# Kernel tuning notes

Measured on AMD Instinct MI355X. Metric: run time of the kernel, lower is better.

The kernel has to match this reference:

```python
import jax, jax.numpy as jnp
import numpy as np

B, T, D = 64, 1024, 512

def setup_inputs() -> dict:
    key = jax.random.key(0)
    ks = jax.random.split(key, 5)
    s_in = 1.0 / np.sqrt(2 * D)
    s_m = 1.0 / np.sqrt(D)
    return {
        "x": jax.random.normal(ks[0], (B, T, D), dtype=jnp.float32),
        "tau_w": jax.random.normal(ks[1], (D, 2 * D), dtype=jnp.float32) * s_in,
        "tau_b": jax.random.normal(ks[2], (D,), dtype=jnp.float32) * s_in,
        "mem_w": jax.random.normal(ks[3], (D, D), dtype=jnp.float32) * s_m,
        "mem_b": jax.random.normal(ks[4], (D,), dtype=jnp.float32) * s_m,
        "threshold": jnp.asarray(0.5, dtype=jnp.float32),
    }

def reference(x, tau_w, tau_b, mem_w, mem_b, threshold):
    b, t, d = x.shape
    dt = x.dtype
    # tau_fc input is cat([xt, tau]); split weight into x-part and tau-part
    Wx = tau_w[:, :d]   # [D, D] acting on xt
    Wt = tau_w[:, d:]   # [D, D] acting on previous tau
    # precompute the parts that depend only on x (dropout=0 -> identity)
    xproj = jnp.einsum('btd,ed->bte', x, Wx) + tau_b      # tau_fc x-contribution
    m = jnp.einsum('btd,ed->bte', x, mem_w) + mem_b       # mem_fc(xt)

    def step(carry, inp):
        v, tau = carry
        xp_t, m_t = inp
        tau = jax.nn.sigmoid(xp_t + tau @ Wt.T)
        alpha = jnp.exp(-1.0 / (tau + 1e-6))
        v = alpha * v + (1.0 - alpha) * m_t
        s = (v >= threshold).astype(dt)
        v = v * (1.0 - s)
        return (v, tau), s

    v0 = jnp.zeros((b, d), dtype=dt)
    tau0 = jnp.ones((b, d), dtype=dt)
    (v, tau), spikes = jax.lax.scan(
        step, (v0, tau0),
        (jnp.swapaxes(xproj, 0, 1), jnp.swapaxes(m, 0, 1)))
    return jnp.swapaxes(spikes, 0, 1), tau, v
```

## Files before the change

kernel.cpp:

```cpp
#include <hip/hip_runtime.h>

#define BB 64
#define TT 1024
#define DD 512
#define BT (BB*TT)

#define SENT 0xFFFFFFFFFFFFFFFFULL
#define TAUG_WORDS (2ULL * 64 * 4 * 192)

typedef float f4 __attribute__((ext_vector_type(4)));

__global__ __launch_bounds__(256, 2) void gemm_kernel(
    const float* __restrict__ x, const float* __restrict__ tau_w,
    const float* __restrict__ tau_b, const float* __restrict__ mem_w,
    const float* __restrict__ mem_b, float* __restrict__ xp, float* __restrict__ mm)
{
    __shared__ float As[32][132];
    __shared__ float Bs[32][68];

    const int tid  = threadIdx.x;
    const int bt0  = blockIdx.x * 128;
    const bool isxp = (blockIdx.y < 8);
    const float* W       = isxp ? tau_w : mem_w;
    const int    wstride = isxp ? 1024 : 512;
    const int    e0      = isxp ? blockIdx.y * 64 : blockIdx.y * 64 - 512;
    const float* bias    = isxp ? tau_b : mem_b;
    float*       dst     = isxp ? xp : mm;

    const int tm = tid & 31, tn = tid >> 5;
    const int lr = tid >> 3, lc = tid & 7;

    float bias_r[8];
#pragma unroll
    for (int ni = 0; ni < 8; ni++) bias_r[ni] = bias[e0 + tn * 8 + ni];

    float acc[4][8] = {};
    float4 pa[4], pb[2];

#pragma unroll
    for (int j = 0; j < 4; j++)
        pa[j] = *(const float4*)(x + (size_t)(bt0 + lr + 32 * j) * DD + lc * 4);
#pragma unroll
    for (int j = 0; j < 2; j++)
        pb[j] = *(const float4*)(W + (size_t)(e0 + lr + 32 * j) * wstride + lc * 4);

    for (int kb = 0; kb < DD; kb += 32) {
#pragma unroll
        for (int j = 0; j < 4; j++) {
            As[lc * 4 + 0][lr + 32 * j] = pa[j].x;
            As[lc * 4 + 1][lr + 32 * j] = pa[j].y;
            As[lc * 4 + 2][lr + 32 * j] = pa[j].z;
            As[lc * 4 + 3][lr + 32 * j] = pa[j].w;
        }
#pragma unroll
        for (int j = 0; j < 2; j++) {
            Bs[lc * 4 + 0][lr + 32 * j] = pb[j].x;
            Bs[lc * 4 + 1][lr + 32 * j] = pb[j].y;
            Bs[lc * 4 + 2][lr + 32 * j] = pb[j].z;
            Bs[lc * 4 + 3][lr + 32 * j] = pb[j].w;
        }
        __syncthreads();
        if (kb + 32 < DD) {
#pragma unroll
            for (int j = 0; j < 4; j++)
                pa[j] = *(const float4*)(x + (size_t)(bt0 + lr + 32 * j) * DD + kb + 32 + lc * 4);
#pragma unroll
            for (int j = 0; j < 2; j++)
                pb[j] = *(const float4*)(W + (size_t)(e0 + lr + 32 * j) * wstride + kb + 32 + lc * 4);
        }
#pragma unroll
        for (int k = 0; k < 32; k++) {
            float4 av  = *(const float4*)&As[k][tm * 4];
            float4 bv0 = *(const float4*)&Bs[k][tn * 8];
            float4 bv1 = *(const float4*)&Bs[k][tn * 8 + 4];
            float a_[4] = {av.x, av.y, av.z, av.w};
            float b_[8] = {bv0.x, bv0.y, bv0.z, bv0.w, bv1.x, bv1.y, bv1.z, bv1.w};
#pragma unroll
            for (int mi = 0; mi < 4; mi++)
#pragma unroll
                for (int ni = 0; ni < 8; ni++)
                    acc[mi][ni] = fmaf(a_[mi], b_[ni], acc[mi][ni]);
        }
        __syncthreads();
    }

#pragma unroll
    for (int mi = 0; mi < 4; mi++) {
        const int row = bt0 + tm * 4 + mi;
        float o[8];
#pragma unroll
        for (int ni = 0; ni < 8; ni++) o[ni] = __fadd_rn(acc[mi][ni], bias_r[ni]);
        float4 s0 = {o[0], o[1], o[2], o[3]};
        float4 s1 = {o[4], o[5], o[6], o[7]};
        *(float4*)(dst + (size_t)row * DD + e0 + tn * 8)     = s0;
        *(float4*)(dst + (size_t)row * DD + e0 + tn * 8 + 4) = s1;
    }
}

__global__ __launch_bounds__(512, 1) void scan_kernel(
    const float* __restrict__ tau_w,
    float* __restrict__ xp_sp,
    const float* __restrict__ mm,
    const float* __restrict__ thrp,
    float* __restrict__ tau_out, float* __restrict__ v_out,
    unsigned long long* __restrict__ taug64)
{
    __shared__ float tau_lds[DD];
    __shared__ float partial[4][128];

    const int wg = blockIdx.x;
    const int b = wg >> 2, p = wg & 3;
    const int tid = threadIdx.x;
    const int w = tid >> 6, lane = tid & 63;
    const int c  = w & 3;
    const int le = ((w >> 2) << 6) + lane;
    const int ge = p * 128 + le;

    float wv[128];
    {
        const float4* wrow = (const float4*)(tau_w + (size_t)ge * 1024 + 512 + c * 128);
#pragma unroll
        for (int j = 0; j < 32; j++) {
            float4 t = wrow[j];
            wv[4 * j + 0] = t.x; wv[4 * j + 1] = t.y;
            wv[4 * j + 2] = t.z; wv[4 * j + 3] = t.w;
        }
    }
#pragma unroll
    for (int j = 0; j < 128; j++) asm volatile("" : "+v"(wv[j]));

    if (tid < DD) tau_lds[tid] = 1.0f;

    const float thr = thrp[0];
    const bool owner = (c == 0);
    float v = 0.0f, tau_keep = 1.0f;
    const size_t baseio = (size_t)b * TT * DD + ge;

    __syncthreads();

    for (int i = 0; i < TT; i++) {
        float xpv = 0.0f, mv = 0.0f;
        if (owner) {
            xpv = xp_sp[baseio + (size_t)i * DD];
            mv  = mm  [baseio + (size_t)i * DD];
        }

        if (i > 0 && tid < 192) {
            const int s = tid >> 6, j = tid & 63;
            const int qsrc = (p + 1 + s) & 3;
            unsigned long long* slot =
                &taug64[(size_t)(i & 1) * (64 * 4 * 192) +
                        (size_t)(b * 4 + p) * 192 + s * 64 + j];
            unsigned long long pk;
            do {
                pk = __hip_atomic_load(slot, __ATOMIC_RELAXED,
                                       __HIP_MEMORY_SCOPE_AGENT);
            } while (pk == SENT);
            __hip_atomic_store(slot, SENT, __ATOMIC_RELAXED,
                               __HIP_MEMORY_SCOPE_AGENT);
            const int e0 = qsrc * 128 + 2 * j;
            tau_lds[e0]     = __uint_as_float((unsigned int)(pk & 0xFFFFFFFFu));
            tau_lds[e0 + 1] = __uint_as_float((unsigned int)(pk >> 32));
        }
        __syncthreads();

        float a0 = 0.f, a1 = 0.f, a2 = 0.f, a3 = 0.f;
        {
            const f4* tl = (const f4*)&tau_lds[c * 128];
#pragma unroll
            for (int j = 0; j < 32; j++) {
                f4 t4 = tl[j];
                a0 = fmaf(wv[4 * j + 0], t4.x, a0);
                a1 = fmaf(wv[4 * j + 1], t4.y, a1);
                a2 = fmaf(wv[4 * j + 2], t4.z, a2);
                a3 = fmaf(wv[4 * j + 3], t4.w, a3);
            }
        }
        partial[c][le] = (a0 + a1) + (a2 + a3);
        __syncthreads();

        if (owner) {
            float dotv = (partial[0][le] + partial[1][le]) +
                         (partial[2][le] + partial[3][le]);
            float z     = __fadd_rn(xpv, dotv);
            float enz   = expf(-z);
            float tau_n = 1.0f / __fadd_rn(1.0f, enz);
            tau_keep = tau_n;

            tau_lds[ge] = tau_n;
            if (i < TT - 1) {
                float pf = __shfl_xor(tau_n, 1);
                if ((lane & 1) == 0) {
                    unsigned long long pk =
                        (unsigned long long)__float_as_uint(tau_n) |
                        ((unsigned long long)__float_as_uint(pf) << 32);
                    const int pl = le >> 1;
#pragma unroll
                    for (int s2 = 0; s2 < 3; s2++) {
                        const int q  = (p + 1 + s2) & 3;
                        const int sr = 2 - s2;
                        __hip_atomic_store(
                            &taug64[(size_t)((i + 1) & 1) * (64 * 4 * 192) +
                                    (size_t)(b * 4 + q) * 192 + sr * 64 + pl],
                            pk, __ATOMIC_RELAXED, __HIP_MEMORY_SCOPE_AGENT);
                    }
                }
            }

            float tpe   = __fadd_rn(tau_n, 1e-6f);
            float alpha = expf(-1.0f / tpe);
            float vn = __fadd_rn(__fmul_rn(alpha, v),
                                 __fmul_rn(__fsub_rn(1.0f, alpha), mv));
            bool s = (vn >= thr);
            xp_sp[baseio + (size_t)i * DD] = s ? 1.0f : 0.0f;
            v = s ? 0.0f : vn;
        }
    }

    if (owner) {
        tau_out[b * DD + ge] = tau_keep;
        v_out  [b * DD + ge] = v;
    }
}

extern "C" void kernel_launch(void* const* d_in, const int* in_sizes, int n_in,
                              void* d_out, int out_size, void* d_ws, size_t ws_size,
                              hipStream_t stream) {
    (void)in_sizes; (void)n_in; (void)out_size; (void)ws_size;
    const float* x     = (const float*)d_in[0];
    const float* tau_w = (const float*)d_in[1];
    const float* tau_b = (const float*)d_in[2];
    const float* mem_w = (const float*)d_in[3];
    const float* mem_b = (const float*)d_in[4];
    const float* thr   = (const float*)d_in[5];
    float* out = (float*)d_out;

    float* mm                   = (float*)d_ws;
    unsigned long long* taug64  = (unsigned long long*)(mm + (size_t)BT * DD);

    hipMemsetAsync(taug64, 0xFF, TAUG_WORDS * sizeof(unsigned long long), stream);

    gemm_kernel<<<dim3(512, 16), 256, 0, stream>>>(x, tau_w, tau_b, mem_w, mem_b,
                                                   out, mm);
    scan_kernel<<<256, 512, 0, stream>>>(tau_w, out, mm, thr,
                                         out + (size_t)BT * DD,
                                         out + (size_t)BT * DD + (size_t)BB * DD,
                                         taug64);
}
```

Baseline: 3.234 ms.

## Replace sentinel mailbox with step-tagged broadcast slots polled by each wave

The cross-workgroup tau exchange changes from per-consumer sentinel mailboxes, which needed three producer stores and a consumer reset store, to one broadcast slot per tau element tagged with the step index. Each remote wave now polls the slots it needs directly and stages the values in a per-wave LDS scratch, so the barrier between the mailbox read and the dot product goes away. A barrier is added at the end of the loop instead. The aim is to cut store traffic and latency on the serial critical path, at the cost of more waves polling global memory at once.

```diff
diff --git a/kernel.cpp b/kernel.cpp
--- a/kernel.cpp
+++ b/kernel.cpp
@@ -5,8 +5,7 @@
 #define DD 512
 #define BT (BB*TT)
 
-#define SENT 0xFFFFFFFFFFFFFFFFULL
-#define TAUG_WORDS (2ULL * 64 * 4 * 192)
+#define TAUG_WORDS (2ULL * 64 * 4 * 128)
 
 typedef float f4 __attribute__((ext_vector_type(4)));
 
@@ -105,8 +104,9 @@
     float* __restrict__ tau_out, float* __restrict__ v_out,
     unsigned long long* __restrict__ taug64)
 {
-    __shared__ float tau_lds[DD];
+    __shared__ __align__(16) float tau_lds[DD];
     __shared__ float partial[4][128];
+    __shared__ __align__(16) float scratch[8][128];
 
     const int wg = blockIdx.x;
     const int b = wg >> 2, p = wg & 3;
@@ -115,6 +115,7 @@
     const int c  = w & 3;
     const int le = ((w >> 2) << 6) + lane;
     const int ge = p * 128 + le;
+    const bool remote = (c != p);
 
     float wv[128];
     {
@@ -145,28 +146,32 @@
             mv  = mm  [baseio + (size_t)i * DD];
         }
 
-        if (i > 0 && tid < 192) {
-            const int s = tid >> 6, j = tid & 63;
-            const int qsrc = (p + 1 + s) & 3;
-            unsigned long long* slot =
-                &taug64[(size_t)(i & 1) * (64 * 4 * 192) +
-                        (size_t)(b * 4 + p) * 192 + s * 64 + j];
-            unsigned long long pk;
+        const float* tsrc;
+        if (i > 0 && remote) {
+            const unsigned tg = (unsigned)i;
+            unsigned long long* sA =
+                &taug64[(size_t)(i & 1) * (64 * 4 * 128) +
+                        (size_t)(b * 4 + c) * 128 + lane];
+            unsigned long long* sB = sA + 64;
+            unsigned long long pkA, pkB;
             do {
-                pk = __hip_atomic_load(slot, __ATOMIC_RELAXED,
-                                       __HIP_MEMORY_SCOPE_AGENT);
-            } while (pk == SENT);
-            __hip_atomic_store(slot, SENT, __ATOMIC_RELAXED,
-                               __HIP_MEMORY_SCOPE_AGENT);
-            const int e0 = qsrc * 128 + 2 * j;
-            tau_lds[e0]     = __uint_as_float((unsigned int)(pk & 0xFFFFFFFFu));
-            tau_lds[e0 + 1] = __uint_as_float((unsigned int)(pk >> 32));
-        }
-        __syncthreads();
+                pkA = __hip_atomic_load(sA, __ATOMIC_RELAXED,
+                                        __HIP_MEMORY_SCOPE_AGENT);
+                pkB = __hip_atomic_load(sB, __ATOMIC_RELAXED,
+                                        __HIP_MEMORY_SCOPE_AGENT);
+            } while ((unsigned)pkA != tg || (unsigned)pkB != tg);
+            scratch[w][lane]      = __uint_as_float((unsigned)(pkA >> 32));
+            scratch[w][lane + 64] = __uint_as_float((unsigned)(pkB >> 32));
+            asm volatile("s_waitcnt lgkmcnt(0)" ::: "memory");
+            __builtin_amdgcn_sched_barrier(0);
+            tsrc = &scratch[w][0];
+        } else {
+            tsrc = &tau_lds[c * 128];
+        }
 
         float a0 = 0.f, a1 = 0.f, a2 = 0.f, a3 = 0.f;
         {
-            const f4* tl = (const f4*)&tau_lds[c * 128];
+            const f4* tl = (const f4*)tsrc;
 #pragma unroll
             for (int j = 0; j < 32; j++) {
                 f4 t4 = tl[j];
@@ -189,22 +194,13 @@
 
             tau_lds[ge] = tau_n;
             if (i < TT - 1) {
-                float pf = __shfl_xor(tau_n, 1);
-                if ((lane & 1) == 0) {
-                    unsigned long long pk =
-                        (unsigned long long)__float_as_uint(tau_n) |
-                        ((unsigned long long)__float_as_uint(pf) << 32);
-                    const int pl = le >> 1;
-#pragma unroll
-                    for (int s2 = 0; s2 < 3; s2++) {
-                        const int q  = (p + 1 + s2) & 3;
-                        const int sr = 2 - s2;
-                        __hip_atomic_store(
-                            &taug64[(size_t)((i + 1) & 1) * (64 * 4 * 192) +
-                                    (size_t)(b * 4 + q) * 192 + sr * 64 + pl],
-                            pk, __ATOMIC_RELAXED, __HIP_MEMORY_SCOPE_AGENT);
-                    }
-                }
+                unsigned long long pk =
+                    ((unsigned long long)__float_as_uint(tau_n) << 32) |
+                    (unsigned long long)(unsigned)(i + 1);
+                __hip_atomic_store(
+                    &taug64[(size_t)((i + 1) & 1) * (64 * 4 * 128) +
+                            (size_t)(b * 4 + p) * 128 + le],
+                    pk, __ATOMIC_RELAXED, __HIP_MEMORY_SCOPE_AGENT);
             }
 
             float tpe   = __fadd_rn(tau_n, 1e-6f);
@@ -215,6 +211,7 @@
             xp_sp[baseio + (size_t)i * DD] = s ? 1.0f : 0.0f;
             v = s ? 0.0f : vn;
         }
+        __syncthreads();
     }
 
     if (owner) {
@@ -238,7 +235,7 @@
     float* mm                   = (float*)d_ws;
     unsigned long long* taug64  = (unsigned long long*)(mm + (size_t)BT * DD);
 
-    hipMemsetAsync(taug64, 0xFF, TAUG_WORDS * sizeof(unsigned long long), stream);
+    hipMemsetAsync(taug64, 0x00, TAUG_WORDS * sizeof(unsigned long long), stream);
 
     gemm_kernel<<<dim3(512, 16), 256, 0, stream>>>(x, tau_w, tau_b, mem_w, mem_b,
                                                    out, mm);
```

After: 3.153 ms. 1.03x faster.
